# Kernel tuning notes

Hardware: AMD Instinct MI355X
Metric: run time of the kernel (lower is better)

Reference implementation:

```python
import jax, jax.numpy as jnp
import numpy as np

TOP_K = 2


def setup_inputs() -> dict:
    key = jax.random.key(0)
    k1, k2 = jax.random.split(key)
    x = jax.random.normal(k1, (4, 4096, 2048), dtype=jnp.float32)
    W = jax.random.normal(k2, (64, 2048), dtype=jnp.float32) * (1.0 / np.sqrt(2048))
    return {"x": x, "W": W}


def reference(x, W):
    B, S, D = x.shape
    E = W.shape[0]
    # logits: [B*S, E] via linear router (no bias)
    flat = x.reshape(-1, D)
    logits = jnp.einsum('td,ed->te', flat, W)
    probs = jax.nn.softmax(logits, axis=-1)
    # eval path: top-k indices
    _, top_k_indices = jax.lax.top_k(probs, TOP_K)          # [T, K]
    # scatter 1s -> mask; scatter gathered probs -> router_probs (== probs*mask)
    router_mask = jax.nn.one_hot(top_k_indices, E, dtype=probs.dtype).sum(axis=-2)  # [T, E]
    router_probs = probs * router_mask
    # normalize (top_k > 1: gradient flows through the sum)
    router_probs = router_probs / router_probs.sum(axis=-1, keepdims=True)
    return (router_mask.reshape(B, S, E),
            top_k_indices.reshape(B, S, TOP_K),
            router_probs.reshape(B, S, E),
            probs.reshape(B, S, E))
```

## Files before the change

### kernel.cpp

```cpp
#include <hip/hip_runtime.h>
#include <math.h>


#define D_DIM 2048
#define E_DIM 64
#define KS 4
#define KSTEPS 16

typedef __bf16 bf16x8 __attribute__((ext_vector_type(8)));
typedef unsigned short us8 __attribute__((ext_vector_type(8)));
typedef float f32x4 __attribute__((ext_vector_type(4)));

static __device__ __forceinline__ unsigned short f2bf(float f) {
    unsigned int u = __float_as_uint(f);
    u += 0x7fffu + ((u >> 16) & 1u);
    return (unsigned short)(u >> 16);
}
static __device__ __forceinline__ float bf2f(unsigned short h) {
    return __uint_as_float(((unsigned int)h) << 16);
}
static __device__ __forceinline__ void split4(const float4 v, ushort4* h, ushort4* l) {
    h->x = f2bf(v.x); l->x = f2bf(v.x - bf2f(h->x));
    h->y = f2bf(v.y); l->y = f2bf(v.y - bf2f(h->y));
    h->z = f2bf(v.z); l->z = f2bf(v.z - bf2f(h->z));
    h->w = f2bf(v.w); l->w = f2bf(v.w - bf2f(h->w));
}

__global__ __launch_bounds__(256, 1) void convert_w(
    const float* __restrict__ W, unsigned short* __restrict__ WB)
{
    int u = blockIdx.x * 256 + threadIdx.x;
    int lane = u & 63;
    int r = u >> 6;
    int h = r & 1;  r >>= 1;
    int n = r & 3;  int sg = r >> 2;
    int E  = n * 16 + (lane & 15);
    int k0 = sg * 32 + (lane >> 4) * 8;
    const float4* src = (const float4*)(W + (size_t)E * D_DIM + k0);
    float4 a = src[0], b = src[1];
    ushort4 ha, la, hb, lb;
    split4(a, &ha, &la);
    split4(b, &hb, &lb);
    us8 out = h ? (us8){la.x, la.y, la.z, la.w, lb.x, lb.y, lb.z, lb.w}
                : (us8){ha.x, ha.y, ha.z, ha.w, hb.x, hb.y, hb.z, hb.w};
    *(us8*)(WB + (size_t)u * 8) = out;
}

__global__ __launch_bounds__(256, 4) void gemm_part(
    const float* __restrict__ x, const unsigned short* __restrict__ WB,
    float* __restrict__ P, int T)
{
    const int tid  = threadIdx.x;
    const int lane = tid & 63;
    const int wv   = tid >> 6;
    const int quad = lane >> 4;
    const int l16  = lane & 15;

    const int ntb = T >> 6;
    const int tb  = blockIdx.x % ntb;
    const int ksl = blockIdx.x / ntb;
    const int t0  = (tb << 6) + wv * 16;
    const int kb  = ksl * (D_DIM / KS);

    const float* xr = x + (size_t)(t0 + l16) * D_DIM + kb + quad * 8;
    const unsigned short* wb = WB + ((size_t)(ksl * KSTEPS) * 512 + lane) * 8;

    f32x4 acc[4];
    #pragma unroll
    for (int n = 0; n < 4; ++n) { f32x4 z = {0.f, 0.f, 0.f, 0.f}; acc[n] = z; }

    float4 xa[3], xb[3];
    bf16x8 Wf[2][4][2];

    xa[0] = *(const float4*)(xr);        xb[0] = *(const float4*)(xr + 4);
    xa[1] = *(const float4*)(xr + 32);   xb[1] = *(const float4*)(xr + 36);
    #pragma unroll
    for (int n = 0; n < 4; ++n)
        #pragma unroll
        for (int h = 0; h < 2; ++h)
            Wf[0][n][h] = *(const bf16x8*)(wb + (n * 2 + h) * 512);

    #pragma unroll
    for (int s = 0; s < KSTEPS; ++s) {
        if (s + 2 < KSTEPS) {
            xa[(s + 2) % 3] = *(const float4*)(xr + (s + 2) * 32);
            xb[(s + 2) % 3] = *(const float4*)(xr + (s + 2) * 32 + 4);
        }
        if (s + 1 < KSTEPS) {
            #pragma unroll
            for (int n = 0; n < 4; ++n)
                #pragma unroll
                for (int h = 0; h < 2; ++h)
                    Wf[(s + 1) & 1][n][h] =
                        *(const bf16x8*)(wb + (size_t)(s + 1) * 4096 + (n * 2 + h) * 512);
        }

        ushort4 h0, l0, h1, l1;
        split4(xa[s % 3], &h0, &l0);
        split4(xb[s % 3], &h1, &l1);
        union { us8 u; bf16x8 b; } ua, ul;
        ua.u = (us8){h0.x, h0.y, h0.z, h0.w, h1.x, h1.y, h1.z, h1.w};
        ul.u = (us8){l0.x, l0.y, l0.z, l0.w, l1.x, l1.y, l1.z, l1.w};

        #pragma unroll
        for (int n = 0; n < 4; ++n) {
            acc[n] = __builtin_amdgcn_mfma_f32_16x16x32_bf16(ua.b, Wf[s & 1][n][0], acc[n], 0, 0, 0);
            acc[n] = __builtin_amdgcn_mfma_f32_16x16x32_bf16(ul.b, Wf[s & 1][n][0], acc[n], 0, 0, 0);
            acc[n] = __builtin_amdgcn_mfma_f32_16x16x32_bf16(ua.b, Wf[s & 1][n][1], acc[n], 0, 0, 0);
        }
    }

    float* Pb = P + ((size_t)ksl * T + t0) * 64;
    #pragma unroll
    for (int n = 0; n < 4; ++n)
        #pragma unroll
        for (int r = 0; r < 4; ++r)
            Pb[(quad * 4 + r) * 64 + n * 16 + l16] = acc[n][r];
}

__global__ __launch_bounds__(256, 4) void reduce_router(
    const float* __restrict__ P, int T,
    float* __restrict__ mask_out, float* __restrict__ idx_out,
    float* __restrict__ rp_out, float* __restrict__ probs_out)
{
    const int tid  = threadIdx.x;
    const int lane = tid & 63;
    const int wv   = tid >> 6;

    for (int i = 0; i < 4; ++i) {
        int t = blockIdx.x * 16 + wv * 4 + i;
        float v = 0.f;
        #pragma unroll
        for (int s = 0; s < KS; ++s)
            v += P[((size_t)s * T + t) * 64 + lane];

        float bv = v; int bi = lane;
        #pragma unroll
        for (int off = 1; off < 64; off <<= 1) {
            float ov = __shfl_xor(bv, off, 64);
            int   oi = __shfl_xor(bi, off, 64);
            bool take = (ov > bv) || (ov == bv && oi < bi);
            bv = take ? ov : bv;
            bi = take ? oi : bi;
        }
        float m = bv; int i1 = bi;

        float p = __expf(v - m);
        float s = p;
        #pragma unroll
        for (int off = 1; off < 64; off <<= 1) s += __shfl_xor(s, off, 64);
        float prob = p / s;

        float v2 = (lane == i1) ? -INFINITY : v;
        float bv2 = v2; int bi2 = lane;
        #pragma unroll
        for (int off = 1; off < 64; off <<= 1) {
            float ov = __shfl_xor(bv2, off, 64);
            int   oi = __shfl_xor(bi2, off, 64);
            bool take = (ov > bv2) || (ov == bv2 && oi < bi2);
            bv2 = take ? ov : bv2;
            bi2 = take ? oi : bi2;
        }
        int i2 = bi2;

        float pd = __shfl(prob, i1, 64) + __shfl(prob, i2, 64);
        bool top = (lane == i1) || (lane == i2);

        mask_out[(size_t)t * 64 + lane]  = top ? 1.f : 0.f;
        rp_out[(size_t)t * 64 + lane]    = top ? prob / pd : 0.f;
        probs_out[(size_t)t * 64 + lane] = prob;
        if (lane == 0) {
            idx_out[(size_t)t * 2]     = (float)i1;
            idx_out[(size_t)t * 2 + 1] = (float)i2;
        }
    }
}

extern "C" void kernel_launch(void* const* d_in, const int* in_sizes, int n_in,
                              void* d_out, int out_size, void* d_ws, size_t ws_size,
                              hipStream_t stream) {
    const float* x = (const float*)d_in[0];
    const float* W = (const float*)d_in[1];
    float* out = (float*)d_out;

    const int T  = in_sizes[0] / D_DIM;
    const int WN = in_sizes[1];

    unsigned short* WB = (unsigned short*)d_ws;
    float* P = (float*)(WB + (size_t)WN * 2);

    float* mask_out  = out;
    float* idx_out   = out + (size_t)T * E_DIM;
    float* rp_out    = idx_out + (size_t)T * 2;
    float* probs_out = rp_out + (size_t)T * E_DIM;

    convert_w<<<dim3((WN * 2) / 8 / 256), dim3(256), 0, stream>>>(W, WB);
    gemm_part<<<dim3((T / 64) * KS), dim3(256), 0, stream>>>(x, WB, P, T);
    reduce_router<<<dim3(T / 16), dim3(256), 0, stream>>>(
        P, T, mask_out, idx_out, rp_out, probs_out);
}
```

Measured before the change: 217.7 us.

## Fuse split-K GEMM and router reduction via shared-memory partial sums

Merges the split-K GEMM and the softmax/top-k reduction into a single kernel. Each 512-thread block has eight waves: two token groups of 16 tokens, each split four ways along K. The waves write their partials to LDS, and the reduction reads and sums them there instead of round-tripping a 4xTx64 partial buffer through global memory. This removes one launch and the partial-sum traffic. In exchange it uses a larger block with 32 KB of shared memory and a barrier, which may lower occupancy and the number of blocks in flight.

```diff
diff --git a/kernel.cpp b/kernel.cpp
--- a/kernel.cpp
+++ b/kernel.cpp
@@ -46,21 +46,24 @@
     *(us8*)(WB + (size_t)u * 8) = out;
 }
 
-__global__ __launch_bounds__(256, 4) void gemm_part(
+__global__ __launch_bounds__(512, 4) void router_fused(
     const float* __restrict__ x, const unsigned short* __restrict__ WB,
-    float* __restrict__ P, int T)
+    float* __restrict__ mask_out, float* __restrict__ idx_out,
+    float* __restrict__ rp_out, float* __restrict__ probs_out)
 {
+    __shared__ __align__(16) float PART[8 * 64 * 16];
+
     const int tid  = threadIdx.x;
     const int lane = tid & 63;
     const int wv   = tid >> 6;
+    const int g    = wv >> 2;
+    const int ksl  = wv & 3;
     const int quad = lane >> 4;
     const int l16  = lane & 15;
 
-    const int ntb = T >> 6;
-    const int tb  = blockIdx.x % ntb;
-    const int ksl = blockIdx.x / ntb;
-    const int t0  = (tb << 6) + wv * 16;
-    const int kb  = ksl * (D_DIM / KS);
+    const int tb = blockIdx.x * 32;
+    const int t0 = tb + g * 16;
+    const int kb = ksl * (D_DIM / KS);
 
     const float* xr = x + (size_t)(t0 + l16) * D_DIM + kb + quad * 8;
     const unsigned short* wb = WB + ((size_t)(ksl * KSTEPS) * 512 + lane) * 8;
@@ -110,29 +113,23 @@
         }
     }
 
-    float* Pb = P + ((size_t)ksl * T + t0) * 64;
     #pragma unroll
     for (int n = 0; n < 4; ++n)
         #pragma unroll
         for (int r = 0; r < 4; ++r)
-            Pb[(quad * 4 + r) * 64 + n * 16 + l16] = acc[n][r];
-}
-
-__global__ __launch_bounds__(256, 4) void reduce_router(
-    const float* __restrict__ P, int T,
-    float* __restrict__ mask_out, float* __restrict__ idx_out,
-    float* __restrict__ rp_out, float* __restrict__ probs_out)
-{
-    const int tid  = threadIdx.x;
-    const int lane = tid & 63;
-    const int wv   = tid >> 6;
+            PART[(wv * 64 + lane) * 16 + n * 4 + r] = acc[n][r];
+    __syncthreads();
 
     for (int i = 0; i < 4; ++i) {
-        int t = blockIdx.x * 16 + wv * 4 + i;
-        float v = 0.f;
-        #pragma unroll
-        for (int s = 0; s < KS; ++s)
-            v += P[((size_t)s * T + t) * 64 + lane];
+        const int t  = wv * 4 + i;
+        const int gg = t >> 4, tt = t & 15;
+        const int e  = lane;
+        const int fo = ((tt >> 2) * 16 + (e & 15)) * 16 + (e >> 4) * 4 + (tt & 3);
+
+        float v = PART[(gg * 4 + 0) * 1024 + fo]
+                + PART[(gg * 4 + 1) * 1024 + fo]
+                + PART[(gg * 4 + 2) * 1024 + fo]
+                + PART[(gg * 4 + 3) * 1024 + fo];
 
         float bv = v; int bi = lane;
         #pragma unroll
@@ -164,14 +161,15 @@
         int i2 = bi2;
 
         float pd = __shfl(prob, i1, 64) + __shfl(prob, i2, 64);
+        const size_t gt = (size_t)(tb + t);
         bool top = (lane == i1) || (lane == i2);
 
-        mask_out[(size_t)t * 64 + lane]  = top ? 1.f : 0.f;
-        rp_out[(size_t)t * 64 + lane]    = top ? prob / pd : 0.f;
-        probs_out[(size_t)t * 64 + lane] = prob;
+        mask_out[gt * 64 + lane]  = top ? 1.f : 0.f;
+        rp_out[gt * 64 + lane]    = top ? prob / pd : 0.f;
+        probs_out[gt * 64 + lane] = prob;
         if (lane == 0) {
-            idx_out[(size_t)t * 2]     = (float)i1;
-            idx_out[(size_t)t * 2 + 1] = (float)i2;
+            idx_out[gt * 2]     = (float)i1;
+            idx_out[gt * 2 + 1] = (float)i2;
         }
     }
 }
@@ -187,7 +185,6 @@
     const int WN = in_sizes[1];
 
     unsigned short* WB = (unsigned short*)d_ws;
-    float* P = (float*)(WB + (size_t)WN * 2);
 
     float* mask_out  = out;
     float* idx_out   = out + (size_t)T * E_DIM;
@@ -195,7 +192,6 @@
     float* probs_out = rp_out + (size_t)T * E_DIM;
 
     convert_w<<<dim3((WN * 2) / 8 / 256), dim3(256), 0, stream>>>(W, WB);
-    gemm_part<<<dim3((T / 64) * KS), dim3(256), 0, stream>>>(x, WB, P, T);
-    reduce_router<<<dim3(T / 16), dim3(256), 0, stream>>>(
-        P, T, mask_out, idx_out, rp_out, probs_out);
+    router_fused<<<dim3(T / 32), dim3(512), 0, stream>>>(
+        x, WB, mask_out, idx_out, rp_out, probs_out);
 }
```

Result: no change. 215.6 us (-1.0%).
